# Kernel tuning notes

Measured on AMD Instinct MI355X. Metric: run time of the kernel, lower is better.

The kernel has to match this reference:

```python
import jax, jax.numpy as jnp
import numpy as np

N = 100000
E = 1600000
IN_DIM = 128
OUT_DIM = 128


def setup_inputs() -> dict:
    key = jax.random.key(0)
    k1, k2, k3, k4, k5 = jax.random.split(key, 5)
    x = jax.random.normal(k1, (N, IN_DIM), dtype=jnp.float32)
    edge_index = jax.random.randint(k2, (2, E), 0, N, dtype=jnp.int64)
    # LayerNorm affine params
    ln_w = jnp.ones((IN_DIM,), dtype=jnp.float32)
    ln_b = jnp.zeros((IN_DIM,), dtype=jnp.float32)
    # SAGEConv params: lin_l (neighbor agg, with bias), lin_r (root, no bias)
    s = 1.0 / np.sqrt(IN_DIM)
    W_l = jax.random.uniform(k3, (OUT_DIM, IN_DIM), dtype=jnp.float32, minval=-s, maxval=s)
    b_l = jax.random.uniform(k4, (OUT_DIM,), dtype=jnp.float32, minval=-s, maxval=s)
    W_r = jax.random.uniform(k5, (OUT_DIM, IN_DIM), dtype=jnp.float32, minval=-s, maxval=s)
    return {"x": x, "edge_index": edge_index, "ln_w": ln_w, "ln_b": ln_b,
            "W_l": W_l, "b_l": b_l, "W_r": W_r}


def _layer_norm(x, w, b, eps=1e-5):
    mu = jnp.mean(x, axis=-1, keepdims=True)
    var = jnp.mean(jnp.square(x - mu), axis=-1, keepdims=True)
    return (x - mu) * jax.lax.rsqrt(var + eps) * w + b


def reference(x, edge_index, ln_w, ln_b, W_l, b_l, W_r):
    # norm -> activation -> dropout(p=0, identity)
    h = jax.nn.relu(_layer_norm(x, ln_w, ln_b))  # [N, in_dim]
    src = edge_index[0]  # message sources (x_j)
    dst = edge_index[1]  # aggregation targets
    # mean aggregation of neighbor features onto target nodes
    agg = jax.ops.segment_sum(h[src], dst, num_segments=N)  # [N, in_dim]
    cnt = jax.ops.segment_sum(jnp.ones((E,), dtype=h.dtype), dst, num_segments=N)
    agg = agg / jnp.maximum(cnt, 1.0)[:, None]
    # SAGEConv: lin_l(agg) + lin_r(h)
    out = agg @ W_l.T + b_l + h @ W_r.T  # [N, out_dim]
    return out
```

## Files before the change

### kernel.cpp

```cpp
#include <hip/hip_runtime.h>

#define N_NODES 100000
#define E_EDGES 1600000
#define DIM     128

#define NB1     391
#define CHUNK   4096
#define NBINS   512
#define NBUCKET 391
#define NBH     (NBINS * NB1)

#define HB_OFF    0
#define WTB_OFF   25600000
#define OFFS_OFF  25665536
#define BHC_OFF   26065600
#define EBG_OFF   26866432
#define BIN_OFF   27667264
#define SRC_OFF   34067264
#define AGGB_OFF  40467264

typedef __attribute__((ext_vector_type(8))) short short8;
typedef __attribute__((ext_vector_type(4))) float floatx4;

__device__ __forceinline__ unsigned bf16pack(float a, float b) {
  unsigned ua = __float_as_uint(a); ua += 0x7fffu + ((ua >> 16) & 1u);
  unsigned ub = __float_as_uint(b); ub += 0x7fffu + ((ub >> 16) & 1u);
  return (ua >> 16) | (ub & 0xffff0000u);
}
__device__ __forceinline__ float2 bf16unpack(unsigned p) {
  return make_float2(__uint_as_float(p << 16), __uint_as_float(p & 0xffff0000u));
}

__global__ __launch_bounds__(256) void k_prep(const float* __restrict__ x,
                                              const float* __restrict__ lw,
                                              const float* __restrict__ lb,
                                              const float* __restrict__ Wl,
                                              const float* __restrict__ Wr,
                                              const int* __restrict__ ei,
                                              unsigned* __restrict__ hb,
                                              unsigned* __restrict__ wtb,
                                              int* __restrict__ bhc) {
  int gid = blockIdx.x * 256 + threadIdx.x;
  int t = threadIdx.x;

  {
    int row  = blockIdx.x * 4 + (t >> 6);
    int lane = t & 63;
    float2 v = ((const float2*)(x + (size_t)row * DIM))[lane];
    float s  = v.x + v.y;
    float sq = v.x * v.x + v.y * v.y;
    #pragma unroll
    for (int off = 32; off > 0; off >>= 1) {
      s  += __shfl_xor(s, off);
      sq += __shfl_xor(sq, off);
    }
    float mu  = s * (1.0f / 128.0f);
    float var = sq * (1.0f / 128.0f) - mu * mu;
    float rs  = rsqrtf(var + 1e-5f);
    float2 w = ((const float2*)lw)[lane];
    float2 b = ((const float2*)lb)[lane];
    float ox = fmaxf((v.x - mu) * rs * w.x + b.x, 0.0f);
    float oy = fmaxf((v.y - mu) * rs * w.y + b.y, 0.0f);
    hb[(size_t)row * 64 + lane] = bf16pack(ox, oy);
  }

  if (gid < 16384) {
    int j2 = gid & 3;
    int q  = (gid >> 2) & 3;
    int c  = (gid >> 4) & 127;
    int kb = gid >> 11;
    int k0 = kb * 32 + q * 8 + j2 * 2;
    int k1 = k0 + 1;
    float v0 = (k0 < 128) ? Wl[c * 128 + k0] : Wr[c * 128 + (k0 - 128)];
    float v1 = (k1 < 128) ? Wl[c * 128 + k1] : Wr[c * 128 + (k1 - 128)];
    wtb[gid] = bf16pack(v0, v1);
  }

  if (blockIdx.x < NB1) {
    __shared__ int h[NBINS];
    h[t] = 0; h[t + 256] = 0;
    __syncthreads();
    const int4* d4p = (const int4*)(ei + E_EDGES);
    #pragma unroll
    for (int u = 0; u < 4; ++u) {
      int i4 = blockIdx.x * (CHUNK / 4) + u * 256 + t;
      if (i4 < E_EDGES / 4) {
        int4 d = d4p[i4];
        atomicAdd(&h[d.x >> 8], 1);
        atomicAdd(&h[d.y >> 8], 1);
        atomicAdd(&h[d.z >> 8], 1);
        atomicAdd(&h[d.w >> 8], 1);
      }
    }
    __syncthreads();
    bhc[t * NB1 + blockIdx.x] = h[t];
    bhc[(t + 256) * NB1 + blockIdx.x] = h[t + 256];
  }
}

__global__ __launch_bounds__(256) void k_binsort(const int* __restrict__ ei,
                                                 const int* __restrict__ bhc,
                                                 int* __restrict__ binned,
                                                 int* __restrict__ ebg) {
  __shared__ int stage[CHUNK];
  __shared__ int hist[NBINS];
  __shared__ int ebase[NBINS];
  __shared__ int cur[NBINS];
  __shared__ int s[256];
  int t  = threadIdx.x;
  int ch = blockIdx.x;

  hist[t]       = bhc[t * NB1 + ch];
  hist[t + 256] = bhc[(t + 256) * NB1 + ch];
  __syncthreads();

  int h0 = hist[2 * t], h1 = hist[2 * t + 1];
  s[t] = h0 + h1;
  __syncthreads();
  #pragma unroll
  for (int off = 1; off < 256; off <<= 1) {
    int xv = (t >= off) ? s[t - off] : 0;
    __syncthreads();
    s[t] += xv;
    __syncthreads();
  }
  int ex = (t > 0) ? s[t - 1] : 0;
  ebase[2 * t] = ex;
  ebase[2 * t + 1] = ex + h0;
  cur[2 * t] = ex;
  cur[2 * t + 1] = ex + h0;
  ebg[(2 * t) * NB1 + ch]     = ex;
  ebg[(2 * t + 1) * NB1 + ch] = ex + h0;
  __syncthreads();

  const int4* s4p = (const int4*)ei;
  const int4* d4p = (const int4*)(ei + E_EDGES);

  #pragma unroll
  for (int u = 0; u < 4; ++u) {
    int i4 = ch * (CHUNK / 4) + u * 256 + t;
    if (i4 < E_EDGES / 4) {
      int4 sv = s4p[i4];
      int4 dv = d4p[i4];
      {
        int bin = dv.x >> 8; int pos = atomicAdd(&cur[bin], 1);
        stage[pos] = sv.x | ((dv.x & 255) << 20);
      }
      {
        int bin = dv.y >> 8; int pos = atomicAdd(&cur[bin], 1);
        stage[pos] = sv.y | ((dv.y & 255) << 20);
      }
      {
        int bin = dv.z >> 8; int pos = atomicAdd(&cur[bin], 1);
        stage[pos] = sv.z | ((dv.z & 255) << 20);
      }
      {
        int bin = dv.w >> 8; int pos = atomicAdd(&cur[bin], 1);
        stage[pos] = sv.w | ((dv.w & 255) << 20);
      }
    }
  }
  __syncthreads();

  int cbase = ch * CHUNK;
  int cnt = E_EDGES - cbase;
  if (cnt > CHUNK) cnt = CHUNK;
  for (int i = t; i < cnt; i += 256)
    binned[cbase + i] = stage[i];
}

__global__ __launch_bounds__(256) void k_csr(const int* __restrict__ bhc,
                                             const int* __restrict__ ebg,
                                             const int* __restrict__ binned,
                                             int* __restrict__ offs,
                                             int* __restrict__ srcidx) {
  __shared__ int h[256];
  __shared__ int s[256];
  __shared__ int cur[256];
  __shared__ int bhcRow[NB1];
  __shared__ int ebgRow[NB1];
  __shared__ int baseSh;
  int t = threadIdx.x;
  int b = blockIdx.x;

  for (int i = t; i < NB1; i += 256) {
    bhcRow[i] = bhc[b * NB1 + i];
    ebgRow[i] = ebg[b * NB1 + i];
  }
  h[t] = 0;
  __syncthreads();

  {
    int p = 0;
    for (int i = t; i < NB1; i += 256) p += ebgRow[i];
    s[t] = p;
    __syncthreads();
    #pragma unroll
    for (int off = 128; off > 0; off >>= 1) {
      if (t < off) s[t] += s[t + off];
      __syncthreads();
    }
    if (t == 0) baseSh = s[0];
    __syncthreads();
  }
  int base = baseSh;

  for (int ch = t; ch < NB1; ch += 256) {
    int st = ch * CHUNK + ebgRow[ch];
    int len = bhcRow[ch];
    for (int k = 0; k < len; ++k)
      atomicAdd(&h[(binned[st + k] >> 20) & 255], 1);
  }
  __syncthreads();

  s[t] = h[t];
  __syncthreads();
  #pragma unroll
  for (int off = 1; off < 256; off <<= 1) {
    int x = (t >= off) ? s[t - off] : 0;
    __syncthreads();
    s[t] += x;
    __syncthreads();
  }
  int excl = (t > 0) ? s[t - 1] : 0;
  cur[t] = excl;
  int node = b * 256 + t;
  if (node < N_NODES) offs[node] = base + excl;
  if (node == N_NODES) offs[N_NODES] = E_EDGES;
  __syncthreads();

  for (int ch = t; ch < NB1; ch += 256) {
    int st = ch * CHUNK + ebgRow[ch];
    int len = bhcRow[ch];
    for (int k = 0; k < len; ++k) {
      int p = binned[st + k];
      int r = atomicAdd(&cur[(p >> 20) & 255], 1);
      srcidx[base + r] = p & 0xFFFFF;
    }
  }
}

__global__ __launch_bounds__(256) void k_gather(const unsigned* __restrict__ hb,
                                                const int* __restrict__ offs,
                                                const int* __restrict__ srcidx,
                                                unsigned* __restrict__ aggb) {
  int wave = threadIdx.x >> 6;
  int lane = threadIdx.x & 63;
  int n0 = blockIdx.x * 8 + wave * 2;
  int n1 = n0 + 1;
  int b0 = __builtin_amdgcn_readfirstlane(offs[n0]);
  int e0 = __builtin_amdgcn_readfirstlane(offs[n0 + 1]);
  int b1 = __builtin_amdgcn_readfirstlane(offs[n1]);
  int e1 = __builtin_amdgcn_readfirstlane(offs[n1 + 1]);
  int m0 = e0 - b0, m1 = e1 - b1;
  int c  = (m0 < m1 ? m0 : m1) & ~7;

  float ax0 = 0.0f, ay0 = 0.0f, ax1 = 0.0f, ay1 = 0.0f;

  for (int j = 0; j < c; j += 8) {
    unsigned p0[8], p1[8];
    #pragma unroll
    for (int i = 0; i < 8; ++i) {
      int s0 = srcidx[b0 + j + i];
      int s1 = srcidx[b1 + j + i];
      p0[i] = hb[(size_t)s0 * 64 + lane];
      p1[i] = hb[(size_t)s1 * 64 + lane];
    }
    #pragma unroll
    for (int i = 0; i < 8; ++i) {
      float2 v0 = bf16unpack(p0[i]);
      float2 v1 = bf16unpack(p1[i]);
      ax0 += v0.x; ay0 += v0.y;
      ax1 += v1.x; ay1 += v1.y;
    }
  }
  for (int j = b0 + c; j < e0; ) {
    int rem = e0 - j;
    if (rem >= 8) {
      unsigned p[8];
      #pragma unroll
      for (int i = 0; i < 8; ++i) p[i] = hb[(size_t)srcidx[j + i] * 64 + lane];
      #pragma unroll
      for (int i = 0; i < 8; ++i) { float2 v = bf16unpack(p[i]); ax0 += v.x; ay0 += v.y; }
      j += 8;
    } else {
      float2 v = bf16unpack(hb[(size_t)srcidx[j] * 64 + lane]);
      ax0 += v.x; ay0 += v.y;
      ++j;
    }
  }
  for (int j = b1 + c; j < e1; ) {
    int rem = e1 - j;
    if (rem >= 8) {
      unsigned p[8];
      #pragma unroll
      for (int i = 0; i < 8; ++i) p[i] = hb[(size_t)srcidx[j + i] * 64 + lane];
      #pragma unroll
      for (int i = 0; i < 8; ++i) { float2 v = bf16unpack(p[i]); ax1 += v.x; ay1 += v.y; }
      j += 8;
    } else {
      float2 v = bf16unpack(hb[(size_t)srcidx[j] * 64 + lane]);
      ax1 += v.x; ay1 += v.y;
      ++j;
    }
  }

  float inv0 = 1.0f / fmaxf((float)m0, 1.0f);
  float inv1 = 1.0f / fmaxf((float)m1, 1.0f);
  aggb[(size_t)n0 * 64 + lane] = bf16pack(ax0 * inv0, ay0 * inv0);
  aggb[(size_t)n1 * 64 + lane] = bf16pack(ax1 * inv1, ay1 * inv1);
}

__global__ __launch_bounds__(256) void k_gemm(const unsigned* __restrict__ aggb,
                                              const unsigned* __restrict__ hb,
                                              const unsigned* __restrict__ wtb,
                                              const float* __restrict__ bl,
                                              float* __restrict__ out) {
  int wave = threadIdx.x >> 6;
  int lane = threadIdx.x & 63;
  int m = lane & 15;
  int q = lane >> 4;
  int r0 = blockIdx.x * 64 + wave * 16;
  int rowA = r0 + m;
  if (rowA > N_NODES - 1) rowA = N_NODES - 1;

  const uint4* ar = (const uint4*)(aggb + (size_t)rowA * 64);
  const uint4* hr = (const uint4*)(hb + (size_t)rowA * 64);
  short8 afrag[8];
  #pragma unroll
  for (int kb = 0; kb < 4; ++kb) {
    uint4 u = ar[kb * 4 + q];
    afrag[kb] = *(short8*)&u;
  }
  #pragma unroll
  for (int kb = 0; kb < 4; ++kb) {
    uint4 u = hr[kb * 4 + q];
    afrag[kb + 4] = *(short8*)&u;
  }

  const uint4* b4 = (const uint4*)wtb;
  #pragma unroll
  for (int ct = 0; ct < 8; ++ct) {
    int c = ct * 16 + m;
    floatx4 acc = {0.0f, 0.0f, 0.0f, 0.0f};
    #pragma unroll
    for (int kb = 0; kb < 8; ++kb) {
      uint4 u = b4[kb * 512 + c * 4 + q];
      short8 bfrag = *(short8*)&u;
      acc = __builtin_amdgcn_mfma_f32_16x16x32_bf16(afrag[kb], bfrag, acc, 0, 0, 0);
    }
    float bias = bl[c];
    #pragma unroll
    for (int reg = 0; reg < 4; ++reg) {
      int r = r0 + q * 4 + reg;
      if (r < N_NODES) out[(size_t)r * DIM + c] = acc[reg] + bias;
    }
  }
}

extern "C" void kernel_launch(void* const* d_in, const int* in_sizes, int n_in,
                              void* d_out, int out_size, void* d_ws, size_t ws_size,
                              hipStream_t stream) {
  const float* x  = (const float*)d_in[0];
  const int*   ei = (const int*)d_in[1];
  const float* lw = (const float*)d_in[2];
  const float* lb = (const float*)d_in[3];
  const float* Wl = (const float*)d_in[4];
  const float* bl = (const float*)d_in[5];
  const float* Wr = (const float*)d_in[6];
  float* out = (float*)d_out;

  char* ws = (char*)d_ws;
  unsigned* hb     = (unsigned*)(ws + HB_OFF);
  unsigned* wtb    = (unsigned*)(ws + WTB_OFF);
  int*      offs   = (int*)(ws + OFFS_OFF);
  int*      bhc    = (int*)(ws + BHC_OFF);
  int*      ebg    = (int*)(ws + EBG_OFF);
  int*      binned = (int*)(ws + BIN_OFF);
  int*      srcidx = (int*)(ws + SRC_OFF);
  unsigned* aggb   = (unsigned*)(ws + AGGB_OFF);

  k_prep<<<N_NODES / 4, 256, 0, stream>>>(x, lw, lb, Wl, Wr, ei, hb, wtb, bhc);
  k_binsort<<<NB1, 256, 0, stream>>>(ei, bhc, binned, ebg);
  k_csr<<<NBUCKET, 256, 0, stream>>>(bhc, ebg, binned, offs, srcidx);
  k_gather<<<N_NODES / 8, 256, 0, stream>>>(hb, offs, srcidx, aggb);
  k_gemm<<<(N_NODES + 63) / 64, 256, 0, stream>>>(aggb, hb, wtb, bl, out);
}
```

Baseline: 254.4 us.

## Fuse edge bin-sort into prep kernel and software-pipeline gather index loads

Merges the separate bin-sort kernel into the prep kernel: each of the first 391 blocks computes its local histogram, scans it in place, and scatters edges into bins, with no second launch or histogram re-read. The gather kernel's main loop now prefetches the next eight source indices while the current feature loads are in flight. This removes a launch and a dependent index-load latency per step. In exchange, every prep block now reserves about 19 KB of shared memory, which can reduce occupancy for the LayerNorm portion.

```diff
diff --git a/kernel.cpp b/kernel.cpp
--- a/kernel.cpp
+++ b/kernel.cpp
@@ -8,7 +8,6 @@
 #define CHUNK   4096
 #define NBINS   512
 #define NBUCKET 391
-#define NBH     (NBINS * NB1)
 
 #define HB_OFF    0
 #define WTB_OFF   25600000
@@ -39,7 +38,13 @@
                                               const int* __restrict__ ei,
                                               unsigned* __restrict__ hb,
                                               unsigned* __restrict__ wtb,
-                                              int* __restrict__ bhc) {
+                                              int* __restrict__ bhc,
+                                              int* __restrict__ ebg,
+                                              int* __restrict__ binned) {
+  __shared__ int h[NBINS];
+  __shared__ int cur[NBINS];
+  __shared__ int s[256];
+  __shared__ int stage[CHUNK];
   int gid = blockIdx.x * 256 + threadIdx.x;
   int t = threadIdx.x;
 
@@ -47,14 +52,14 @@
     int row  = blockIdx.x * 4 + (t >> 6);
     int lane = t & 63;
     float2 v = ((const float2*)(x + (size_t)row * DIM))[lane];
-    float s  = v.x + v.y;
+    float sx  = v.x + v.y;
     float sq = v.x * v.x + v.y * v.y;
     #pragma unroll
     for (int off = 32; off > 0; off >>= 1) {
-      s  += __shfl_xor(s, off);
+      sx += __shfl_xor(sx, off);
       sq += __shfl_xor(sq, off);
     }
-    float mu  = s * (1.0f / 128.0f);
+    float mu  = sx * (1.0f / 128.0f);
     float var = sq * (1.0f / 128.0f) - mu * mu;
     float rs  = rsqrtf(var + 1e-5f);
     float2 w = ((const float2*)lw)[lane];
@@ -77,13 +82,14 @@
   }
 
   if (blockIdx.x < NB1) {
-    __shared__ int h[NBINS];
+    int ch = blockIdx.x;
     h[t] = 0; h[t + 256] = 0;
     __syncthreads();
+    const int4* s4p = (const int4*)ei;
     const int4* d4p = (const int4*)(ei + E_EDGES);
     #pragma unroll
     for (int u = 0; u < 4; ++u) {
-      int i4 = blockIdx.x * (CHUNK / 4) + u * 256 + t;
+      int i4 = ch * (CHUNK / 4) + u * 256 + t;
       if (i4 < E_EDGES / 4) {
         int4 d = d4p[i4];
         atomicAdd(&h[d.x >> 8], 1);
@@ -93,80 +99,55 @@
       }
     }
     __syncthreads();
-    bhc[t * NB1 + blockIdx.x] = h[t];
-    bhc[(t + 256) * NB1 + blockIdx.x] = h[t + 256];
-  }
-}
-
-__global__ __launch_bounds__(256) void k_binsort(const int* __restrict__ ei,
-                                                 const int* __restrict__ bhc,
-                                                 int* __restrict__ binned,
-                                                 int* __restrict__ ebg) {
-  __shared__ int stage[CHUNK];
-  __shared__ int hist[NBINS];
-  __shared__ int ebase[NBINS];
-  __shared__ int cur[NBINS];
-  __shared__ int s[256];
-  int t  = threadIdx.x;
-  int ch = blockIdx.x;
-
-  hist[t]       = bhc[t * NB1 + ch];
-  hist[t + 256] = bhc[(t + 256) * NB1 + ch];
-  __syncthreads();
-
-  int h0 = hist[2 * t], h1 = hist[2 * t + 1];
-  s[t] = h0 + h1;
-  __syncthreads();
-  #pragma unroll
-  for (int off = 1; off < 256; off <<= 1) {
-    int xv = (t >= off) ? s[t - off] : 0;
-    __syncthreads();
-    s[t] += xv;
-    __syncthreads();
-  }
-  int ex = (t > 0) ? s[t - 1] : 0;
-  ebase[2 * t] = ex;
-  ebase[2 * t + 1] = ex + h0;
-  cur[2 * t] = ex;
-  cur[2 * t + 1] = ex + h0;
-  ebg[(2 * t) * NB1 + ch]     = ex;
-  ebg[(2 * t + 1) * NB1 + ch] = ex + h0;
-  __syncthreads();
-
-  const int4* s4p = (const int4*)ei;
-  const int4* d4p = (const int4*)(ei + E_EDGES);
-
-  #pragma unroll
-  for (int u = 0; u < 4; ++u) {
-    int i4 = ch * (CHUNK / 4) + u * 256 + t;
-    if (i4 < E_EDGES / 4) {
-      int4 sv = s4p[i4];
-      int4 dv = d4p[i4];
-      {
-        int bin = dv.x >> 8; int pos = atomicAdd(&cur[bin], 1);
-        stage[pos] = sv.x | ((dv.x & 255) << 20);
-      }
-      {
-        int bin = dv.y >> 8; int pos = atomicAdd(&cur[bin], 1);
-        stage[pos] = sv.y | ((dv.y & 255) << 20);
-      }
-      {
-        int bin = dv.z >> 8; int pos = atomicAdd(&cur[bin], 1);
-        stage[pos] = sv.z | ((dv.z & 255) << 20);
-      }
-      {
-        int bin = dv.w >> 8; int pos = atomicAdd(&cur[bin], 1);
-        stage[pos] = sv.w | ((dv.w & 255) << 20);
-      }
-    }
-  }
-  __syncthreads();
-
-  int cbase = ch * CHUNK;
-  int cnt = E_EDGES - cbase;
-  if (cnt > CHUNK) cnt = CHUNK;
-  for (int i = t; i < cnt; i += 256)
-    binned[cbase + i] = stage[i];
+    int h0 = h[2 * t], h1 = h[2 * t + 1];
+    bhc[(2 * t) * NB1 + ch]     = h0;
+    bhc[(2 * t + 1) * NB1 + ch] = h1;
+    s[t] = h0 + h1;
+    __syncthreads();
+    #pragma unroll
+    for (int off = 1; off < 256; off <<= 1) {
+      int xv = (t >= off) ? s[t - off] : 0;
+      __syncthreads();
+      s[t] += xv;
+      __syncthreads();
+    }
+    int ex = (t > 0) ? s[t - 1] : 0;
+    cur[2 * t] = ex;
+    cur[2 * t + 1] = ex + h0;
+    ebg[(2 * t) * NB1 + ch]     = ex;
+    ebg[(2 * t + 1) * NB1 + ch] = ex + h0;
+    __syncthreads();
+    #pragma unroll
+    for (int u = 0; u < 4; ++u) {
+      int i4 = ch * (CHUNK / 4) + u * 256 + t;
+      if (i4 < E_EDGES / 4) {
+        int4 sv = s4p[i4];
+        int4 dv = d4p[i4];
+        {
+          int bin = dv.x >> 8; int pos = atomicAdd(&cur[bin], 1);
+          stage[pos] = sv.x | ((dv.x & 255) << 20);
+        }
+        {
+          int bin = dv.y >> 8; int pos = atomicAdd(&cur[bin], 1);
+          stage[pos] = sv.y | ((dv.y & 255) << 20);
+        }
+        {
+          int bin = dv.z >> 8; int pos = atomicAdd(&cur[bin], 1);
+          stage[pos] = sv.z | ((dv.z & 255) << 20);
+        }
+        {
+          int bin = dv.w >> 8; int pos = atomicAdd(&cur[bin], 1);
+          stage[pos] = sv.w | ((dv.w & 255) << 20);
+        }
+      }
+    }
+    __syncthreads();
+    int cbase = ch * CHUNK;
+    int cnt = E_EDGES - cbase;
+    if (cnt > CHUNK) cnt = CHUNK;
+    for (int i = t; i < cnt; i += 256)
+      binned[cbase + i] = stage[i];
+  }
 }
 
 __global__ __launch_bounds__(256) void k_csr(const int* __restrict__ bhc,
@@ -257,21 +238,34 @@
 
   float ax0 = 0.0f, ay0 = 0.0f, ax1 = 0.0f, ay1 = 0.0f;
 
-  for (int j = 0; j < c; j += 8) {
-    unsigned p0[8], p1[8];
+  if (c > 0) {
+    int sA[8], sB[8];
     #pragma unroll
     for (int i = 0; i < 8; ++i) {
-      int s0 = srcidx[b0 + j + i];
-      int s1 = srcidx[b1 + j + i];
-      p0[i] = hb[(size_t)s0 * 64 + lane];
-      p1[i] = hb[(size_t)s1 * 64 + lane];
-    }
-    #pragma unroll
-    for (int i = 0; i < 8; ++i) {
-      float2 v0 = bf16unpack(p0[i]);
-      float2 v1 = bf16unpack(p1[i]);
-      ax0 += v0.x; ay0 += v0.y;
-      ax1 += v1.x; ay1 += v1.y;
+      sA[i] = srcidx[b0 + i];
+      sB[i] = srcidx[b1 + i];
+    }
+    for (int j = 0; j < c; j += 8) {
+      unsigned p0[8], p1[8];
+      #pragma unroll
+      for (int i = 0; i < 8; ++i) {
+        p0[i] = hb[(size_t)sA[i] * 64 + lane];
+        p1[i] = hb[(size_t)sB[i] * 64 + lane];
+      }
+      if (j + 8 < c) {
+        #pragma unroll
+        for (int i = 0; i < 8; ++i) {
+          sA[i] = srcidx[b0 + j + 8 + i];
+          sB[i] = srcidx[b1 + j + 8 + i];
+        }
+      }
+      #pragma unroll
+      for (int i = 0; i < 8; ++i) {
+        float2 v0 = bf16unpack(p0[i]);
+        float2 v1 = bf16unpack(p1[i]);
+        ax0 += v0.x; ay0 += v0.y;
+        ax1 += v1.x; ay1 += v1.y;
+      }
     }
   }
   for (int j = b0 + c; j < e0; ) {
@@ -380,8 +374,7 @@
   int*      srcidx = (int*)(ws + SRC_OFF);
   unsigned* aggb   = (unsigned*)(ws + AGGB_OFF);
 
-  k_prep<<<N_NODES / 4, 256, 0, stream>>>(x, lw, lb, Wl, Wr, ei, hb, wtb, bhc);
-  k_binsort<<<NB1, 256, 0, stream>>>(ei, bhc, binned, ebg);
+  k_prep<<<N_NODES / 4, 256, 0, stream>>>(x, lw, lb, Wl, Wr, ei, hb, wtb, bhc, ebg, binned);
   k_csr<<<NBUCKET, 256, 0, stream>>>(bhc, ebg, binned, offs, srcidx);
   k_gather<<<N_NODES / 8, 256, 0, stream>>>(hb, offs, srcidx, aggb);
   k_gemm<<<(N_NODES + 63) / 64, 256, 0, stream>>>(aggb, hb, wtb, bl, out);
```

After: 249.0 us. 2.1% less time.
